# Kernel tuning notes

Hardware: AMD Instinct MI355X
Metric: run time of the kernel (lower is better)

The kernel has to match this reference:

```python
import jax, jax.numpy as jnp
import numpy as np

N, D, E, EDGE_DIM = 8192, 64, 262144, 4


def setup_inputs() -> dict:
    key = jax.random.key(0)
    k1, k2, k3, k4, k5, k6 = jax.random.split(key, 6)
    mag = jax.random.uniform(k1, (N, D), dtype=jnp.float32)
    phase = jax.random.normal(k2, (N, D), dtype=jnp.float32)
    edge_index = jax.random.randint(k3, (2, E), 0, N, dtype=jnp.int64)
    edge_attr = jax.random.normal(k4, (E, EDGE_DIM), dtype=jnp.float32)
    # nn.Linear(edge_dim, hidden_dim): weight [hidden_dim, edge_dim], bias [hidden_dim]
    bound = 1.0 / np.sqrt(EDGE_DIM)
    W = jax.random.uniform(k5, (D, EDGE_DIM), minval=-bound, maxval=bound, dtype=jnp.float32)
    b = jax.random.uniform(k6, (D,), minval=-bound, maxval=bound, dtype=jnp.float32)
    return {"mag": mag, "phase": phase, "edge_index": edge_index,
            "edge_attr": edge_attr, "W": W, "b": b}


def reference(mag, phase, edge_index, edge_attr, W, b):
    # score_ij = sum_d mag_i[d]*mag_j[d]*cos(phase_i[d]-phase_j[d])
    # Via cos(a-b) = cos a cos b + sin a sin b -> two [N,D]@[D,N] matmuls,
    # avoiding the O(N^2 D) intermediate while computing identical math.
    c = mag * jnp.cos(phase)  # [N, D]
    s = mag * jnp.sin(phase)  # [N, D]
    scores = c @ c.T + s @ s.T  # [N, N]
    # edge bias: edge_bias[src, dst] = sum_h Linear(edge_attr)[e, h]
    edge_scores = (edge_attr @ W.T + b).sum(axis=-1)  # [E]
    bias = jnp.zeros((mag.shape[0], mag.shape[0]), dtype=scores.dtype)
    bias = bias.at[edge_index[0], edge_index[1]].set(edge_scores)
    scores = scores + bias
    attn = jax.nn.softmax(scores, axis=1)  # [N, N]
    new_mag = attn @ mag  # [N, D]
    new_phase = attn @ phase  # [N, D]
    return new_mag, new_phase
```

## Files before the change

### kernel.cpp

```cpp
#include <hip/hip_runtime.h>
#include <hip/hip_bf16.h>
#include <cstdint>

#define N_NODES 8192
#define DDIM    64
#define DX      128
#define NEDGE   262144
#define BR      128
#define BC      64
#define SPLITS  8
#define TILES   (N_NODES / BC / SPLITS)
#define RCAP    64
#define MSHIFT  66.0f

typedef float f32x16 __attribute__((ext_vector_type(16)));
typedef short short8 __attribute__((ext_vector_type(8)));

__device__ __forceinline__ short f2bf(float f) {
    union { float f; uint32_t u; } v; v.f = f;
    uint32_t u = v.u;
    uint32_t r = (u + 0x7FFFu + ((u >> 16) & 1u)) >> 16;
    return (short)r;
}
__device__ __forceinline__ float bf2f(short s) {
    union { uint32_t u; float f; } v;
    v.u = ((uint32_t)(uint16_t)s) << 16;
    return v.f;
}

__global__ void cpa_prep_all(const float* __restrict__ mag, const float* __restrict__ phase,
                             const int* __restrict__ ei, const float* __restrict__ ea,
                             const float* __restrict__ W, const float* __restrict__ b,
                             short* __restrict__ Xbf, short* __restrict__ Ybt,
                             float* __restrict__ es, int* __restrict__ cnt,
                             int* __restrict__ keys) {
    __shared__ short tile[64][65];
    __shared__ float wsb[5];
    const int blk = blockIdx.x;
    const int tid = threadIdx.x;
    if (blk < 2048) {
        int idx = blk * 256 + tid;
        int i = idx >> 6, d = idx & 63;
        float m = mag[idx], p = phase[idx];
        Xbf[i * DX + d]      = f2bf(m * __cosf(p));
        Xbf[i * DX + 64 + d] = f2bf(m * __sinf(p));
    } else if (blk < 2304) {
        int bb = blk - 2048;
        int bi = bb >> 1;
        int bc = bb & 1;
        int i0 = bi * 64;
        const float* src = bc ? phase : mag;
        for (int itr = 0; itr < 16; ++itr) {
            int idx = tid + itr * 256;
            int ii = idx >> 6, cc = idx & 63;
            tile[ii][cc] = f2bf(src[(size_t)(i0 + ii) * 64 + cc]);
        }
        __syncthreads();
        for (int itr = 0; itr < 16; ++itr) {
            int idx = tid + itr * 256;
            int cc = idx >> 6, ii = idx & 63;
            Ybt[(size_t)(bc * 64 + cc) * N_NODES + i0 + ii] = tile[ii][cc];
        }
    } else {
        if (tid < 64) {
            float w0 = W[tid * 4 + 0], w1 = W[tid * 4 + 1];
            float w2 = W[tid * 4 + 2], w3 = W[tid * 4 + 3];
            float bb = b[tid];
            #pragma unroll
            for (int o = 32; o > 0; o >>= 1) {
                w0 += __shfl_down(w0, o);
                w1 += __shfl_down(w1, o);
                w2 += __shfl_down(w2, o);
                w3 += __shfl_down(w3, o);
                bb += __shfl_down(bb, o);
            }
            if (tid == 0) { wsb[0] = w0; wsb[1] = w1; wsb[2] = w2; wsb[3] = w3; wsb[4] = bb; }
        }
        __syncthreads();
        int e = (blk - 2304) * 256 + tid;
        float4 a = *(const float4*)(ea + (size_t)e * 4);
        es[e] = a.x * wsb[0] + a.y * wsb[1] + a.z * wsb[2] + a.w * wsb[3] + wsb[4];
        int src = ei[e];
        int dst = ei[NEDGE + e];
        int pos = atomicAdd(&cnt[src], 1);
        if (pos < RCAP) keys[src * RCAP + pos] = (dst << 18) | e;
    }
}

__global__ __launch_bounds__(256) void cpa_sortrows(const int* __restrict__ cnt,
                                                    int* __restrict__ keys) {
    int row  = blockIdx.x * 4 + (threadIdx.x >> 6);
    int lane = threadIdx.x & 63;
    int len  = min(cnt[row], RCAP);
    int base = row * RCAP;
    int v = (lane < len) ? keys[base + lane] : 0x7FFFFFFF;

    #pragma unroll
    for (int k = 2; k <= 64; k <<= 1) {
        #pragma unroll
        for (int j = k >> 1; j >= 1; j >>= 1) {
            int p = __shfl_xor(v, j);
            bool asc = (lane & k) == 0;
            bool low = (lane & j) == 0;
            v = (low == asc) ? min(v, p) : max(v, p);
        }
    }
    int nxt = __shfl_down(v, 1);
    bool dead = (lane + 1 < len) && ((v >> 18) == (nxt >> 18));
    if (lane < len) keys[base + lane] = v | (dead ? 0x80000000 : 0);
}

__global__ __launch_bounds__(512, 4) void cpa_flash(
    const short* __restrict__ Xbf, const short* __restrict__ Ybt,
    const float* __restrict__ es, const int* __restrict__ keys,
    const int* __restrict__ cnt,
    float* __restrict__ lsplit, short* __restrict__ Opart)
{
    __shared__ short Xj[BC][136];
    __shared__ short Yt[DX][72];
    __shared__ short Pl[BR][72];

    const int tid  = threadIdx.x;
    const int lane = tid & 63;
    const int w    = tid >> 6;
    const int l31  = lane & 31;
    const int lh   = lane >> 5;
    const int rg   = w >> 1;
    const int cg   = w & 1;
    const int ocg0 = (w & 1) * 2;

    const int ib = blockIdx.x;
    const int split = blockIdx.y;
    const int i0 = ib * BR;
    const int jstart = split * (N_NODES / SPLITS);

    short8 afrag[8];
    #pragma unroll
    for (int kf = 0; kf < 8; ++kf)
        afrag[kf] = *(const short8*)(Xbf + (size_t)(i0 + rg * 32 + l31) * DX + kf * 16 + lh * 8);

    short8 ones;
    #pragma unroll
    for (int j = 0; j < 8; ++j) ones[j] = (short)0x3F80;

    int cur = 0, rend = 0;
    if (lane < 32) {
        int i = i0 + rg * 32 + l31;
        cur = i * RCAP;
        rend = cur + min(cnt[i], RCAP);
        while (cur < rend) {
            int k = keys[cur];
            if (((k >> 18) & 0x1FFF) >= jstart) break;
            ++cur;
        }
    }

    f32x16 O0, O1, lC;
    #pragma unroll
    for (int r = 0; r < 16; ++r) { O0[r] = 0.f; O1[r] = 0.f; lC[r] = 0.f; }

    for (int tt = 0; tt < TILES; ++tt) {
        const int j0 = jstart + tt * BC;
        for (int itr = 0; itr < 2; ++itr) {
            int idx = tid + itr * 512;
            int r = idx >> 4;
            int c8 = (idx & 15) << 3;
            *(int4*)(&Xj[r][c8]) = *(const int4*)(Xbf + (size_t)(j0 + r) * DX + c8);
        }
        for (int itr = 0; itr < 2; ++itr) {
            int idx = tid + itr * 512;
            int n = idx >> 3;
            int k8 = (idx & 7) << 3;
            *(int4*)(&Yt[n][k8]) = *(const int4*)(Ybt + (size_t)n * N_NODES + j0 + k8);
        }
        __syncthreads();

        f32x16 S;
        #pragma unroll
        for (int r = 0; r < 16; ++r) S[r] = 0.f;
        #pragma unroll
        for (int kf = 0; kf < 8; ++kf) {
            short8 bfrag = *(const short8*)&Xj[cg * 32 + l31][kf * 16 + lh * 8];
            S = __builtin_amdgcn_mfma_f32_32x32x16_bf16(afrag[kf], bfrag, S, 0, 0, 0);
        }
        #pragma unroll
        for (int r = 0; r < 16; ++r) {
            int rowl = 4 * lh + (r & 3) + 8 * (r >> 2);
            Pl[rg * 32 + rowl][cg * 32 + l31] = f2bf(__expf(S[r] - MSHIFT));
        }
        if (lane < 32) {
            const int jend = j0 + BC;
            const int wlo = j0 + cg * 32;
            int c = cur;
            while (c < rend) {
                int k = keys[c];
                int dst = (k >> 18) & 0x1FFF;
                if (dst >= jend) break;
                ++c;
                if (k >= 0) {
                    unsigned cl = (unsigned)(dst - wlo);
                    if (cl < 32u) {
                        short* p = &Pl[rg * 32 + l31][cg * 32 + (int)cl];
                        *p = f2bf(bf2f(*p) * __expf(es[k & 0x3FFFF]));
                    }
                }
            }
            cur = c;
        }
        __syncthreads();

        #pragma unroll
        for (int ks = 0; ks < 4; ++ks) {
            short8 pa  = *(const short8*)&Pl[rg * 32 + l31][ks * 16 + lh * 8];
            short8 yb0 = *(const short8*)&Yt[ocg0 * 32 + l31][ks * 16 + lh * 8];
            short8 yb1 = *(const short8*)&Yt[(ocg0 + 1) * 32 + l31][ks * 16 + lh * 8];
            O0 = __builtin_amdgcn_mfma_f32_32x32x16_bf16(pa, yb0, O0, 0, 0, 0);
            O1 = __builtin_amdgcn_mfma_f32_32x32x16_bf16(pa, yb1, O1, 0, 0, 0);
            if (!(w & 1))
                lC = __builtin_amdgcn_mfma_f32_32x32x16_bf16(pa, ones, lC, 0, 0, 0);
        }
        __syncthreads();
    }

    #pragma unroll
    for (int r = 0; r < 16; ++r) {
        int row = rg * 32 + 4 * lh + (r & 3) + 8 * (r >> 2);
        size_t base = ((size_t)split * N_NODES + i0 + row) * DX;
        Opart[base + ocg0 * 32 + l31]       = f2bf(O0[r]);
        Opart[base + (ocg0 + 1) * 32 + l31] = f2bf(O1[r]);
    }
    if (!(w & 1) && l31 == 0) {
        #pragma unroll
        for (int r = 0; r < 16; ++r) {
            int row = rg * 32 + 4 * lh + (r & 3) + 8 * (r >> 2);
            lsplit[(size_t)split * N_NODES + i0 + row] = lC[r];
        }
    }
}

__global__ void cpa_merge(const float* __restrict__ lsplit, const short* __restrict__ Opart,
                          float* __restrict__ out) {
    int gid = blockIdx.x * 256 + threadIdx.x;
    int i = gid >> 7;
    int c = gid & 127;
    float den = 0.f, num = 0.f;
    #pragma unroll
    for (int s = 0; s < SPLITS; ++s) {
        den += lsplit[(size_t)s * N_NODES + i];
        num += bf2f(Opart[((size_t)s * N_NODES + i) * DX + c]);
    }
    float val = num / den;
    if (c < 64) out[(size_t)i * 64 + c] = val;
    else        out[(size_t)N_NODES * 64 + (size_t)i * 64 + (c - 64)] = val;
}

extern "C" void kernel_launch(void* const* d_in, const int* in_sizes, int n_in,
                              void* d_out, int out_size, void* d_ws, size_t ws_size,
                              hipStream_t stream)
{
    const float* mag   = (const float*)d_in[0];
    const float* phase = (const float*)d_in[1];
    const int*   ei    = (const int*)d_in[2];
    const float* ea    = (const float*)d_in[3];
    const float* W     = (const float*)d_in[4];
    const float* b     = (const float*)d_in[5];
    float* out = (float*)d_out;

    char* ws = (char*)d_ws;
    short* Xbf    = (short*)(ws + 0);
    short* Ybt    = (short*)(ws + 2097152);
    float* es     = (float*)(ws + 4194304);
    int*   keys   = (int*)  (ws + 5242880);
    int*   cnt    = (int*)  (ws + 7340032);
    float* lsplit = (float*)(ws + 7373056);
    short* Opart  = (short*)(ws + 7635200);

    hipMemsetAsync(cnt, 0, N_NODES * sizeof(int), stream);
    cpa_prep_all<<<2048 + 256 + NEDGE / 256, 256, 0, stream>>>(mag, phase, ei, ea, W, b,
                                                               Xbf, Ybt, es, cnt, keys);
    cpa_sortrows<<<N_NODES / 4, 256, 0, stream>>>(cnt, keys);
    cpa_flash<<<dim3(N_NODES / BR, SPLITS), 512, 0, stream>>>(Xbf, Ybt, es, keys, cnt,
                                                              lsplit, Opart);
    cpa_merge<<<N_NODES * DX / 256, 256, 0, stream>>>(lsplit, Opart, out);
}
```

Baseline: 167.4 us.

## Restructure flash kernel with async LDS loads, transposed S, and register-resident P

Rewrites the attention inner loop. X_j and Y tiles now stream into swizzled LDS through global_load_lds, with the X_j tile double-buffered and prefetched one tile ahead. S is computed transposed so each lane owns a row, letting edge-bias factors multiply P in registers instead of via read-modify-write to LDS. The exp of the edge scores moves into the prep kernel. P is packed to bf16 in registers and exchanged between wave pairs through a small LDS swap buffer, and the row sum is accumulated in scalar registers instead of through a ones-MFMA. This targets LDS traffic, sync stalls and redundant MFMAs, at the cost of more complex data movement and added shuffle and select work.

```diff
diff --git a/kernel.cpp b/kernel.cpp
--- a/kernel.cpp
+++ b/kernel.cpp
@@ -26,6 +26,19 @@
     union { uint32_t u; float f; } v;
     v.u = ((uint32_t)(uint16_t)s) << 16;
     return v.f;
+}
+__device__ __forceinline__ unsigned cvtpk_bf16(float lo, float hi) {
+    unsigned r;
+    asm("v_cvt_pk_bf16_f32 %0, %1, %2" : "=v"(r) : "v"(lo), "v"(hi));
+    return r;
+}
+__device__ __forceinline__ float bfsum2(unsigned w) {
+    return bf2f((short)(w & 0xFFFFu)) + bf2f((short)(w >> 16));
+}
+__device__ __forceinline__ void gload_lds16(const short* g, short* l) {
+    __builtin_amdgcn_global_load_lds(
+        (const __attribute__((address_space(1))) unsigned int*)g,
+        (__attribute__((address_space(3))) unsigned int*)l, 16, 0, 0);
 }
 
 __global__ void cpa_prep_all(const float* __restrict__ mag, const float* __restrict__ phase,
@@ -79,7 +92,7 @@
         __syncthreads();
         int e = (blk - 2304) * 256 + tid;
         float4 a = *(const float4*)(ea + (size_t)e * 4);
-        es[e] = a.x * wsb[0] + a.y * wsb[1] + a.z * wsb[2] + a.w * wsb[3] + wsb[4];
+        es[e] = __expf(a.x * wsb[0] + a.y * wsb[1] + a.z * wsb[2] + a.w * wsb[3] + wsb[4]);
         int src = ei[e];
         int dst = ei[NEDGE + e];
         int pos = atomicAdd(&cnt[src], 1);
@@ -116,125 +129,175 @@
     const int* __restrict__ cnt,
     float* __restrict__ lsplit, short* __restrict__ Opart)
 {
-    __shared__ short Xj[BC][136];
-    __shared__ short Yt[DX][72];
-    __shared__ short Pl[BR][72];
+    __shared__ short XjT[2][64][128];
+    __shared__ short Yt[128][64];
+    __shared__ unsigned swp[4][2][2][64][4];
 
     const int tid  = threadIdx.x;
     const int lane = tid & 63;
     const int w    = tid >> 6;
     const int l31  = lane & 31;
     const int lh   = lane >> 5;
-    const int rg   = w >> 1;
-    const int cg   = w & 1;
-    const int ocg0 = (w & 1) * 2;
+    const int ig   = w >> 1;
+    const int jg   = w & 1;
 
     const int ib = blockIdx.x;
     const int split = blockIdx.y;
     const int i0 = ib * BR;
     const int jstart = split * (N_NODES / SPLITS);
 
-    short8 afrag[8];
+    short8 xi[8];
     #pragma unroll
     for (int kf = 0; kf < 8; ++kf)
-        afrag[kf] = *(const short8*)(Xbf + (size_t)(i0 + rg * 32 + l31) * DX + kf * 16 + lh * 8);
-
-    short8 ones;
-    #pragma unroll
-    for (int j = 0; j < 8; ++j) ones[j] = (short)0x3F80;
-
-    int cur = 0, rend = 0;
-    if (lane < 32) {
-        int i = i0 + rg * 32 + l31;
-        cur = i * RCAP;
-        rend = cur + min(cnt[i], RCAP);
-        while (cur < rend) {
-            int k = keys[cur];
-            if (((k >> 18) & 0x1FFF) >= jstart) break;
-            ++cur;
-        }
-    }
-
-    f32x16 O0, O1, lC;
-    #pragma unroll
-    for (int r = 0; r < 16; ++r) { O0[r] = 0.f; O1[r] = 0.f; lC[r] = 0.f; }
-
+        xi[kf] = *(const short8*)(Xbf + (size_t)(i0 + ig * 32 + l31) * DX + kf * 16 + lh * 8);
+
+    const int xr0 = w * 8 + (lane >> 4);
+    const int xc  = lane & 15;
+    const int xo0 = (xc ^ (xr0 & 15)) << 3;
+    const int xr1 = xr0 + 4;
+    const int xo1 = (xc ^ (xr1 & 15)) << 3;
+    const int yr0 = w * 16 + (lane >> 3);
+    const int yc  = lane & 7;
+    const int yo0 = (yc ^ (yr0 & 7)) << 3;
+    const int yr1 = yr0 + 8;
+    const int yo1 = (yc ^ (yr1 & 7)) << 3;
+
+    {
+        const short* xsrc = Xbf + (size_t)jstart * DX;
+        gload_lds16(xsrc + (size_t)xr0 * DX + xo0, &XjT[0][w * 8][0]);
+        gload_lds16(xsrc + (size_t)xr1 * DX + xo1, &XjT[0][w * 8 + 4][0]);
+    }
+
+    const int myrow = i0 + ig * 32 + l31;
+    int cur  = myrow * RCAP;
+    int rend = cur + min(cnt[myrow], RCAP);
+    int kcur = 0;
+    while (cur < rend) {
+        kcur = keys[cur];
+        if (((kcur >> 18) & 0x1FFF) >= jstart) break;
+        ++cur;
+    }
+
+    f32x16 O0, O1;
+    float lacc = 0.f;
+    #pragma unroll
+    for (int r = 0; r < 16; ++r) { O0[r] = 0.f; O1[r] = 0.f; }
+
+    __syncthreads();
+
+    int buf = 0;
     for (int tt = 0; tt < TILES; ++tt) {
         const int j0 = jstart + tt * BC;
-        for (int itr = 0; itr < 2; ++itr) {
-            int idx = tid + itr * 512;
-            int r = idx >> 4;
-            int c8 = (idx & 15) << 3;
-            *(int4*)(&Xj[r][c8]) = *(const int4*)(Xbf + (size_t)(j0 + r) * DX + c8);
-        }
-        for (int itr = 0; itr < 2; ++itr) {
-            int idx = tid + itr * 512;
-            int n = idx >> 3;
-            int k8 = (idx & 7) << 3;
-            *(int4*)(&Yt[n][k8]) = *(const int4*)(Ybt + (size_t)n * N_NODES + j0 + k8);
-        }
-        __syncthreads();
+
+        gload_lds16(Ybt + (size_t)yr0 * N_NODES + j0 + yo0, &Yt[w * 16][0]);
+        gload_lds16(Ybt + (size_t)yr1 * N_NODES + j0 + yo1, &Yt[w * 16 + 8][0]);
+        if (tt + 1 < TILES) {
+            const short* xsrc = Xbf + (size_t)(j0 + BC) * DX;
+            gload_lds16(xsrc + (size_t)xr0 * DX + xo0, &XjT[buf ^ 1][w * 8][0]);
+            gload_lds16(xsrc + (size_t)xr1 * DX + xo1, &XjT[buf ^ 1][w * 8 + 4][0]);
+        }
 
         f32x16 S;
         #pragma unroll
         for (int r = 0; r < 16; ++r) S[r] = 0.f;
+        const int rr = jg * 32 + l31;
+        __builtin_amdgcn_s_setprio(1);
         #pragma unroll
         for (int kf = 0; kf < 8; ++kf) {
-            short8 bfrag = *(const short8*)&Xj[cg * 32 + l31][kf * 16 + lh * 8];
-            S = __builtin_amdgcn_mfma_f32_32x32x16_bf16(afrag[kf], bfrag, S, 0, 0, 0);
-        }
-        #pragma unroll
-        for (int r = 0; r < 16; ++r) {
-            int rowl = 4 * lh + (r & 3) + 8 * (r >> 2);
-            Pl[rg * 32 + rowl][cg * 32 + l31] = f2bf(__expf(S[r] - MSHIFT));
-        }
-        if (lane < 32) {
-            const int jend = j0 + BC;
-            const int wlo = j0 + cg * 32;
-            int c = cur;
-            while (c < rend) {
-                int k = keys[c];
-                int dst = (k >> 18) & 0x1FFF;
-                if (dst >= jend) break;
-                ++c;
-                if (k >= 0) {
-                    unsigned cl = (unsigned)(dst - wlo);
-                    if (cl < 32u) {
-                        short* p = &Pl[rg * 32 + l31][cg * 32 + (int)cl];
-                        *p = f2bf(bf2f(*p) * __expf(es[k & 0x3FFFF]));
-                    }
+            const int co = kf * 2 + lh;
+            short8 af = *(const short8*)&XjT[buf][rr][(co ^ (rr & 15)) << 3];
+            S = __builtin_amdgcn_mfma_f32_32x32x16_bf16(af, xi[kf], S, 0, 0, 0);
+        }
+        __builtin_amdgcn_s_setprio(0);
+
+        f32x16 p;
+        #pragma unroll
+        for (int r = 0; r < 16; ++r) p[r] = __expf(S[r] - MSHIFT);
+
+        {
+            const int wlo  = j0 + jg * 32;
+            const int wend = wlo + 32;
+            while (cur < rend) {
+                int dst = (kcur >> 18) & 0x1FFF;
+                if (dst >= wend) break;
+                int kk = kcur;
+                ++cur;
+                if (cur < rend) kcur = keys[cur];
+                int jl = dst - wlo;
+                if (kk >= 0 && jl >= 0 && ((jl >> 2) & 1) == lh) {
+                    float m = es[kk & 0x3FFFF];
+                    int sel = (jl & 3) | ((jl >> 3) << 2);
+                    #pragma unroll
+                    for (int r = 0; r < 16; ++r)
+                        if (r == sel) p[r] *= m;
                 }
             }
-            cur = c;
-        }
+        }
+
+        unsigned c0 = cvtpk_bf16(p[0], p[1]),   c1 = cvtpk_bf16(p[2], p[3]);
+        unsigned c2 = cvtpk_bf16(p[4], p[5]),   c3 = cvtpk_bf16(p[6], p[7]);
+        unsigned c4 = cvtpk_bf16(p[8], p[9]),   c5 = cvtpk_bf16(p[10], p[11]);
+        unsigned c6 = cvtpk_bf16(p[12], p[13]), c7 = cvtpk_bf16(p[14], p[15]);
+        unsigned t0 = __shfl_xor(c0, 32), t2 = __shfl_xor(c2, 32);
+        unsigned t1 = __shfl_xor(c1, 32), t3 = __shfl_xor(c3, 32);
+        unsigned t4 = __shfl_xor(c4, 32), t6 = __shfl_xor(c6, 32);
+        unsigned t5 = __shfl_xor(c5, 32), t7 = __shfl_xor(c7, 32);
+        union FU { unsigned u[4]; short8 s; int4 v; };
+        FU F0, F1;
+        F0.u[0] = lh ? t2 : c0;  F0.u[1] = lh ? t3 : c1;
+        F0.u[2] = lh ? c2 : t0;  F0.u[3] = lh ? c3 : t1;
+        F1.u[0] = lh ? t6 : c4;  F1.u[1] = lh ? t7 : c5;
+        F1.u[2] = lh ? c6 : t4;  F1.u[3] = lh ? c7 : t5;
+
+        lacc += bfsum2(F0.u[0]) + bfsum2(F0.u[1]) + bfsum2(F0.u[2]) + bfsum2(F0.u[3]);
+        lacc += bfsum2(F1.u[0]) + bfsum2(F1.u[1]) + bfsum2(F1.u[2]) + bfsum2(F1.u[3]);
+
+        *(int4*)&swp[ig][jg][0][lane][0] = F0.v;
+        *(int4*)&swp[ig][jg][1][lane][0] = F1.v;
+
         __syncthreads();
 
-        #pragma unroll
-        for (int ks = 0; ks < 4; ++ks) {
-            short8 pa  = *(const short8*)&Pl[rg * 32 + l31][ks * 16 + lh * 8];
-            short8 yb0 = *(const short8*)&Yt[ocg0 * 32 + l31][ks * 16 + lh * 8];
-            short8 yb1 = *(const short8*)&Yt[(ocg0 + 1) * 32 + l31][ks * 16 + lh * 8];
-            O0 = __builtin_amdgcn_mfma_f32_32x32x16_bf16(pa, yb0, O0, 0, 0, 0);
-            O1 = __builtin_amdgcn_mfma_f32_32x32x16_bf16(pa, yb1, O1, 0, 0, 0);
-            if (!(w & 1))
-                lC = __builtin_amdgcn_mfma_f32_32x32x16_bf16(pa, ones, lC, 0, 0, 0);
-        }
+        short8 own0 = F0.s, own1 = F1.s;
+        short8 oth0 = *(const short8*)&swp[ig][jg ^ 1][0][lane][0];
+        short8 oth1 = *(const short8*)&swp[ig][jg ^ 1][1][lane][0];
+
+        const int fA = jg * 64 + l31;
+        const int fB = fA + 32;
+        __builtin_amdgcn_s_setprio(1);
+        #pragma unroll
+        for (int sl = 0; sl < 2; ++sl) {
+            short8 ao = sl ? own1 : own0;
+            short8 at = sl ? oth1 : oth0;
+            const int co_o = jg * 4 + sl * 2 + lh;
+            const int co_t = (jg ^ 1) * 4 + sl * 2 + lh;
+            short8 b0o = *(const short8*)&Yt[fA][(co_o ^ (fA & 7)) << 3];
+            short8 b0t = *(const short8*)&Yt[fA][(co_t ^ (fA & 7)) << 3];
+            short8 b1o = *(const short8*)&Yt[fB][(co_o ^ (fB & 7)) << 3];
+            short8 b1t = *(const short8*)&Yt[fB][(co_t ^ (fB & 7)) << 3];
+            O0 = __builtin_amdgcn_mfma_f32_32x32x16_bf16(ao, b0o, O0, 0, 0, 0);
+            O0 = __builtin_amdgcn_mfma_f32_32x32x16_bf16(at, b0t, O0, 0, 0, 0);
+            O1 = __builtin_amdgcn_mfma_f32_32x32x16_bf16(ao, b1o, O1, 0, 0, 0);
+            O1 = __builtin_amdgcn_mfma_f32_32x32x16_bf16(at, b1t, O1, 0, 0, 0);
+        }
+        __builtin_amdgcn_s_setprio(0);
+
         __syncthreads();
-    }
+        buf ^= 1;
+    }
+
+    lacc += __shfl_xor(lacc, 32);
+    float* lmbuf = (float*)&swp[0][0][0][0][0];
+    if (jg == 1 && lane < 32) lmbuf[ig * 32 + l31] = lacc;
+    __syncthreads();
+    if (jg == 0 && lane < 32)
+        lsplit[(size_t)split * N_NODES + i0 + ig * 32 + l31] = lacc + lmbuf[ig * 32 + l31];
 
     #pragma unroll
     for (int r = 0; r < 16; ++r) {
-        int row = rg * 32 + 4 * lh + (r & 3) + 8 * (r >> 2);
+        int row = ig * 32 + 4 * lh + (r & 3) + 8 * (r >> 2);
         size_t base = ((size_t)split * N_NODES + i0 + row) * DX;
-        Opart[base + ocg0 * 32 + l31]       = f2bf(O0[r]);
-        Opart[base + (ocg0 + 1) * 32 + l31] = f2bf(O1[r]);
-    }
-    if (!(w & 1) && l31 == 0) {
-        #pragma unroll
-        for (int r = 0; r < 16; ++r) {
-            int row = rg * 32 + 4 * lh + (r & 3) + 8 * (r >> 2);
-            lsplit[(size_t)split * N_NODES + i0 + row] = lC[r];
-        }
+        Opart[base + jg * 64 + l31]      = f2bf(O0[r]);
+        Opart[base + jg * 64 + 32 + l31] = f2bf(O1[r]);
     }
 }
 
```

Result: no change. 169.1 us (+1.0%).
